# Performance work log

Hardware: AMD Instinct MI355X
Metric: run time of the kernel (lower is better)

Reference implementation:

```python
import jax, jax.numpy as jnp
import numpy as np

NUM_CLASSES = 1000
BATCH = 65536
TEMPERATURE = 1.0
SMOOTHING = 0.1


def setup_inputs() -> dict:
    key = jax.random.key(0)
    k1, k2, k3 = jax.random.split(key, 3)
    x = jax.random.normal(k1, (BATCH, NUM_CLASSES), dtype=jnp.float32)
    class_avg = jax.random.normal(k2, (NUM_CLASSES, NUM_CLASSES), dtype=jnp.float32)
    target = jax.random.randint(k3, (BATCH,), 0, NUM_CLASSES, dtype=jnp.int64)
    return {"x": x, "class_avg": class_avg, "target": target}


def reference(x, class_avg, target):
    C = class_avg.shape[0]
    # class_avg = softmax(class_avg / T) over last dim
    A = jax.nn.softmax(class_avg / TEMPERATURE, axis=-1)  # [C, C]
    # per-class off-diagonal mass: sum over row minus diagonal
    sums = A.sum(axis=-1) - jnp.diagonal(A)  # [C]
    # per-class smoothing matrix S[t, j] = smoothing * (1 - A[t, j]) / sums[t], S[t, t] = 1 - smoothing
    S = SMOOTHING * (1.0 - A) / sums[:, None]  # [C, C]
    diag_idx = jnp.arange(C)
    S = S.at[diag_idx, diag_idx].set(1.0 - SMOOTHING)
    # gather the per-sample smoothing rows (replaces the nested Python loop)
    sm = S[target]  # [B, C]
    logprobs = jax.nn.log_softmax(x, axis=-1)  # [B, C]
    loss = -(logprobs * sm).sum(axis=-1)  # [B]
    return loss.mean()
```

## Files before the change

### kernel.cpp

```cpp
#include <hip/hip_runtime.h>
#include <math.h>

constexpr int C = 1000;
constexpr int B = 65536;
constexpr float SMOOTH = 0.1f;
constexpr int SPW = 2;
constexpr int WPB = 4;
constexpr int LBLK = B / (WPB * SPW);

typedef float f4 __attribute__((ext_vector_type(4)));

__device__ inline float wave_reduce_sum(float v) {
    #pragma unroll
    for (int off = 32; off > 0; off >>= 1)
        v += __shfl_xor(v, off, 64);
    return v;
}
__device__ inline void wave_reduce_sum4(float& a, float& b, float& c, float& d) {
    #pragma unroll
    for (int off = 32; off > 0; off >>= 1) {
        float ta = __shfl_xor(a, off, 64);
        float tb = __shfl_xor(b, off, 64);
        float tc = __shfl_xor(c, off, 64);
        float td = __shfl_xor(d, off, 64);
        a += ta; b += tb; c += tc; d += td;
    }
}
__device__ inline float block_reduce_sum(float v, float* sm) {
    v = wave_reduce_sum(v);
    int wave = threadIdx.x >> 6, lane = threadIdx.x & 63;
    if (lane == 0) sm[wave] = v;
    __syncthreads();
    float r = (sm[0] + sm[1]) + (sm[2] + sm[3]);
    __syncthreads();
    return r;
}

__global__ __launch_bounds__(256) void smooth_kernel(
        const float* __restrict__ ca, float* __restrict__ S,
        float* __restrict__ Srow) {
    int wave = threadIdx.x >> 6, lane = threadIdx.x & 63;
    int t = blockIdx.x * 4 + wave;
    const f4* row = (const f4*)(ca + (size_t)t * C);
    bool lastl = lane < (250 - 192);

    f4 e[4];
    e[0] = row[lane];
    e[1] = row[lane + 64];
    e[2] = row[lane + 128];
    e[3] = lastl ? row[lane + 192]
                 : f4{-INFINITY, -INFINITY, -INFINITY, -INFINITY};

    float zl = 0.f;
    #pragma unroll
    for (int k = 0; k < 4; k++) {
        e[k].x = __expf(e[k].x);
        e[k].y = __expf(e[k].y);
        e[k].z = __expf(e[k].z);
        e[k].w = __expf(e[k].w);
        zl += (e[k].x + e[k].y) + (e[k].z + e[k].w);
    }
    float z = wave_reduce_sum(zl);
    float inv_z = 1.0f / z;

    int q = t >> 2, owner = q & 63, kk = q >> 6, comp = t & 3;
    f4 av = (kk == 0) ? e[0] : (kk == 1) ? e[1] : (kk == 2) ? e[2] : e[3];
    float cand = (comp == 0) ? av.x : (comp == 1) ? av.y
               : (comp == 2) ? av.z : av.w;
    float ediag = __shfl(cand, owner, 64);

    float sums = (z - ediag) * inv_z;
    float coef = SMOOTH / sums;
    f4* Srt = (f4*)(S + (size_t)t * C);
    float srow_l = 0.f;
    #pragma unroll
    for (int k = 0; k < 3; k++) {
        int jb = (lane + k * 64) * 4;
        f4 s;
        s.x = (jb + 0 == t) ? (1.0f - SMOOTH) : (1.0f - e[k].x * inv_z) * coef;
        s.y = (jb + 1 == t) ? (1.0f - SMOOTH) : (1.0f - e[k].y * inv_z) * coef;
        s.z = (jb + 2 == t) ? (1.0f - SMOOTH) : (1.0f - e[k].z * inv_z) * coef;
        s.w = (jb + 3 == t) ? (1.0f - SMOOTH) : (1.0f - e[k].w * inv_z) * coef;
        Srt[lane + k * 64] = s;
        srow_l += (s.x + s.y) + (s.z + s.w);
    }
    if (lastl) {
        int jb = (lane + 192) * 4;
        f4 s;
        s.x = (jb + 0 == t) ? (1.0f - SMOOTH) : (1.0f - e[3].x * inv_z) * coef;
        s.y = (jb + 1 == t) ? (1.0f - SMOOTH) : (1.0f - e[3].y * inv_z) * coef;
        s.z = (jb + 2 == t) ? (1.0f - SMOOTH) : (1.0f - e[3].z * inv_z) * coef;
        s.w = (jb + 3 == t) ? (1.0f - SMOOTH) : (1.0f - e[3].w * inv_z) * coef;
        Srt[lane + 192] = s;
        srow_l += (s.x + s.y) + (s.z + s.w);
    }
    float srow = wave_reduce_sum(srow_l);
    if (lane == 0) Srow[t] = srow;
}

__global__ __launch_bounds__(256) void loss_kernel(
        const float* __restrict__ x, const float* __restrict__ S,
        const float* __restrict__ Srow, const int* __restrict__ tgt,
        float* __restrict__ partials) {
    int wave = threadIdx.x >> 6, lane = threadIdx.x & 63;
    int b0 = (blockIdx.x * WPB + wave) * SPW;
    bool lastl = lane < (250 - 192);

    int t0 = tgt[b0], t1 = tgt[b0 + 1];
    float ss0 = Srow[t0], ss1 = Srow[t1];
    const f4* xr0 = (const f4*)(x + (size_t)b0 * C);
    const f4* xr1 = (const f4*)(x + (size_t)(b0 + 1) * C);
    const f4* sr0 = (const f4*)(S + (size_t)t0 * C);
    const f4* sr1 = (const f4*)(S + (size_t)t1 * C);

    f4 xa0 = __builtin_nontemporal_load(xr0 + lane);
    f4 xa1 = __builtin_nontemporal_load(xr0 + lane + 64);
    f4 xa2 = __builtin_nontemporal_load(xr0 + lane + 128);
    f4 xa3 = lastl ? __builtin_nontemporal_load(xr0 + lane + 192)
                   : f4{-INFINITY, -INFINITY, -INFINITY, -INFINITY};
    f4 sa0 = sr0[lane], sa1 = sr0[lane + 64], sa2 = sr0[lane + 128];
    f4 sa3 = lastl ? sr0[lane + 192] : f4{0.f, 0.f, 0.f, 0.f};

    f4 xb0 = __builtin_nontemporal_load(xr1 + lane);
    f4 xb1 = __builtin_nontemporal_load(xr1 + lane + 64);
    f4 xb2 = __builtin_nontemporal_load(xr1 + lane + 128);
    f4 xb3 = lastl ? __builtin_nontemporal_load(xr1 + lane + 192)
                   : f4{-INFINITY, -INFINITY, -INFINITY, -INFINITY};
    f4 sb0 = sr1[lane], sb1 = sr1[lane + 64], sb2 = sr1[lane + 128];
    f4 sb3 = lastl ? sr1[lane + 192] : f4{0.f, 0.f, 0.f, 0.f};

    float z0 = 0.f, d0 = 0.f, z1 = 0.f, d1 = 0.f;

    {
        z0 += __expf(xa0.x) + __expf(xa0.y) + __expf(xa0.z) + __expf(xa0.w);
        z0 += __expf(xa1.x) + __expf(xa1.y) + __expf(xa1.z) + __expf(xa1.w);
        z0 += __expf(xa2.x) + __expf(xa2.y) + __expf(xa2.z) + __expf(xa2.w);
        z0 += __expf(xa3.x) + __expf(xa3.y) + __expf(xa3.z) + __expf(xa3.w);
        d0 = fmaf(sa0.x, xa0.x, d0); d0 = fmaf(sa0.y, xa0.y, d0);
        d0 = fmaf(sa0.z, xa0.z, d0); d0 = fmaf(sa0.w, xa0.w, d0);
        d0 = fmaf(sa1.x, xa1.x, d0); d0 = fmaf(sa1.y, xa1.y, d0);
        d0 = fmaf(sa1.z, xa1.z, d0); d0 = fmaf(sa1.w, xa1.w, d0);
        d0 = fmaf(sa2.x, xa2.x, d0); d0 = fmaf(sa2.y, xa2.y, d0);
        d0 = fmaf(sa2.z, xa2.z, d0); d0 = fmaf(sa2.w, xa2.w, d0);
        f4 xf = lastl ? xa3 : f4{0.f, 0.f, 0.f, 0.f};
        d0 = fmaf(sa3.x, xf.x, d0); d0 = fmaf(sa3.y, xf.y, d0);
        d0 = fmaf(sa3.z, xf.z, d0); d0 = fmaf(sa3.w, xf.w, d0);
    }
    {
        z1 += __expf(xb0.x) + __expf(xb0.y) + __expf(xb0.z) + __expf(xb0.w);
        z1 += __expf(xb1.x) + __expf(xb1.y) + __expf(xb1.z) + __expf(xb1.w);
        z1 += __expf(xb2.x) + __expf(xb2.y) + __expf(xb2.z) + __expf(xb2.w);
        z1 += __expf(xb3.x) + __expf(xb3.y) + __expf(xb3.z) + __expf(xb3.w);
        d1 = fmaf(sb0.x, xb0.x, d1); d1 = fmaf(sb0.y, xb0.y, d1);
        d1 = fmaf(sb0.z, xb0.z, d1); d1 = fmaf(sb0.w, xb0.w, d1);
        d1 = fmaf(sb1.x, xb1.x, d1); d1 = fmaf(sb1.y, xb1.y, d1);
        d1 = fmaf(sb1.z, xb1.z, d1); d1 = fmaf(sb1.w, xb1.w, d1);
        d1 = fmaf(sb2.x, xb2.x, d1); d1 = fmaf(sb2.y, xb2.y, d1);
        d1 = fmaf(sb2.z, xb2.z, d1); d1 = fmaf(sb2.w, xb2.w, d1);
        f4 xf = lastl ? xb3 : f4{0.f, 0.f, 0.f, 0.f};
        d1 = fmaf(sb3.x, xf.x, d1); d1 = fmaf(sb3.y, xf.y, d1);
        d1 = fmaf(sb3.z, xf.z, d1); d1 = fmaf(sb3.w, xf.w, d1);
    }

    wave_reduce_sum4(z0, z1, d0, d1);

    float lb = __logf(z0) * ss0 - d0 + __logf(z1) * ss1 - d1;

    __shared__ float wacc[4];
    if (lane == 0) wacc[wave] = lb;
    __syncthreads();
    if (threadIdx.x == 0)
        partials[blockIdx.x] = (wacc[0] + wacc[1]) + (wacc[2] + wacc[3]);
}

__global__ __launch_bounds__(256) void reduce_kernel(
        const float* __restrict__ partials, float* __restrict__ out) {
    __shared__ float sm[4];
    const f4* p4 = (const f4*)partials;
    float s = 0.f;
    #pragma unroll
    for (int k = 0; k < 8; k++) {
        f4 v = p4[threadIdx.x + k * 256];
        s += (v.x + v.y) + (v.z + v.w);
    }
    s = block_reduce_sum(s, sm);
    if (threadIdx.x == 0) out[0] = s * (1.0f / (float)B);
}

extern "C" void kernel_launch(void* const* d_in, const int* in_sizes, int n_in,
                              void* d_out, int out_size, void* d_ws, size_t ws_size,
                              hipStream_t stream) {
    const float* x   = (const float*)d_in[0];
    const float* ca  = (const float*)d_in[1];
    const int*   tgt = (const int*)d_in[2];
    float* out = (float*)d_out;

    float* S        = (float*)d_ws;
    float* Srow     = S + (size_t)C * C;
    float* partials = Srow + C;

    smooth_kernel<<<C / 4, 256, 0, stream>>>(ca, S, Srow);
    loss_kernel<<<LBLK, 256, 0, stream>>>(x, S, Srow, tgt, partials);
    reduce_kernel<<<1, 256, 0, stream>>>(partials, out);
}
```

Measured before the change: 340.1 us.

## Bucket samples by target class so each wave reuses one smoothing row

Adds histogram, prefix-scan and scatter kernels that group sample indices by target class. The loss kernel then assigns 8 waves per class, loads that class's smoothing row into registers once, and loops over that class's samples. This removes the per-sample gather of a 4KB S row, which is largely L2 traffic. In exchange it adds four small serialized launches, atomics, and an indirect, non-sequential access pattern over x, and load balance now depends on how many samples each class has.

```diff
diff --git a/kernel.cpp b/kernel.cpp
--- a/kernel.cpp
+++ b/kernel.cpp
@@ -4,17 +4,26 @@
 constexpr int C = 1000;
 constexpr int B = 65536;
 constexpr float SMOOTH = 0.1f;
-constexpr int SPW = 2;
-constexpr int WPB = 4;
-constexpr int LBLK = B / (WPB * SPW);
+constexpr int WPC = 8;
+constexpr int NW = C * WPC;
+constexpr int NWPAD = 8192;
 
 typedef float f4 __attribute__((ext_vector_type(4)));
+#define NTLOAD(p) __builtin_nontemporal_load(p)
 
 __device__ inline float wave_reduce_sum(float v) {
     #pragma unroll
     for (int off = 32; off > 0; off >>= 1)
         v += __shfl_xor(v, off, 64);
     return v;
+}
+__device__ inline void wave_reduce_sum2(float& a, float& b) {
+    #pragma unroll
+    for (int off = 32; off > 0; off >>= 1) {
+        float ta = __shfl_xor(a, off, 64);
+        float tb = __shfl_xor(b, off, 64);
+        a += ta; b += tb;
+    }
 }
 __device__ inline void wave_reduce_sum4(float& a, float& b, float& c, float& d) {
     #pragma unroll
@@ -34,6 +43,75 @@
     float r = (sm[0] + sm[1]) + (sm[2] + sm[3]);
     __syncthreads();
     return r;
+}
+
+
+__global__ __launch_bounds__(256) void zero_kernel(int* __restrict__ counts) {
+    #pragma unroll
+    for (int k = 0; k < 4; k++) {
+        int idx = threadIdx.x + k * 256;
+        if (idx < C) counts[idx] = 0;
+    }
+}
+
+__global__ __launch_bounds__(256) void hist_kernel(const int* __restrict__ tgt,
+                                                   int* __restrict__ counts) {
+    __shared__ int lh[C];
+    for (int idx = threadIdx.x; idx < C; idx += 256) lh[idx] = 0;
+    __syncthreads();
+    int base = blockIdx.x * 1024 + threadIdx.x;
+    #pragma unroll
+    for (int k = 0; k < 4; k++)
+        atomicAdd(&lh[tgt[base + k * 256]], 1);
+    __syncthreads();
+    for (int idx = threadIdx.x; idx < C; idx += 256) {
+        int v = lh[idx];
+        if (v) atomicAdd(&counts[idx], v);
+    }
+}
+
+__global__ __launch_bounds__(256) void prefix_kernel(const int* __restrict__ counts,
+                                                     int* __restrict__ offs,
+                                                     int* __restrict__ cursor) {
+    __shared__ int ts[256];
+    int tid = threadIdx.x;
+    int c[4];
+    int s = 0;
+    #pragma unroll
+    for (int k = 0; k < 4; k++) {
+        int idx = tid * 4 + k;
+        c[k] = (idx < C) ? counts[idx] : 0;
+        s += c[k];
+    }
+    ts[tid] = s;
+    __syncthreads();
+    for (int off = 1; off < 256; off <<= 1) {
+        int v = (tid >= off) ? ts[tid - off] : 0;
+        __syncthreads();
+        ts[tid] += v;
+        __syncthreads();
+    }
+    int base = (tid > 0) ? ts[tid - 1] : 0;
+    #pragma unroll
+    for (int k = 0; k < 4; k++) {
+        int idx = tid * 4 + k;
+        if (idx < C) { offs[idx] = base; cursor[idx] = base; }
+        base += c[k];
+    }
+    if (tid == 255) offs[C] = ts[255];
+}
+
+__global__ __launch_bounds__(256) void scatter_kernel(const int* __restrict__ tgt,
+                                                      int* __restrict__ cursor,
+                                                      int* __restrict__ order) {
+    int base = blockIdx.x * 1024 + threadIdx.x;
+    #pragma unroll
+    for (int k = 0; k < 4; k++) {
+        int b = base + k * 256;
+        int t = tgt[b];
+        int pos = atomicAdd(&cursor[t], 1);
+        order[pos] = b;
+    }
 }
 
 __global__ __launch_bounds__(256) void smooth_kernel(
@@ -98,79 +176,72 @@
     if (lane == 0) Srow[t] = srow;
 }
 
+__device__ inline void sample_zd(const f4* __restrict__ xr, int lane, bool lastl,
+                                 const f4& s0, const f4& s1, const f4& s2,
+                                 const f4& s3, float& z, float& d) {
+    f4 x0 = NTLOAD(xr + lane);
+    f4 x1 = NTLOAD(xr + lane + 64);
+    f4 x2 = NTLOAD(xr + lane + 128);
+    f4 x3 = lastl ? NTLOAD(xr + lane + 192)
+                  : f4{-INFINITY, -INFINITY, -INFINITY, -INFINITY};
+    z = __expf(x0.x) + __expf(x0.y) + __expf(x0.z) + __expf(x0.w)
+      + __expf(x1.x) + __expf(x1.y) + __expf(x1.z) + __expf(x1.w)
+      + __expf(x2.x) + __expf(x2.y) + __expf(x2.z) + __expf(x2.w)
+      + __expf(x3.x) + __expf(x3.y) + __expf(x3.z) + __expf(x3.w);
+    float dd = 0.f;
+    dd = fmaf(s0.x, x0.x, dd); dd = fmaf(s0.y, x0.y, dd);
+    dd = fmaf(s0.z, x0.z, dd); dd = fmaf(s0.w, x0.w, dd);
+    dd = fmaf(s1.x, x1.x, dd); dd = fmaf(s1.y, x1.y, dd);
+    dd = fmaf(s1.z, x1.z, dd); dd = fmaf(s1.w, x1.w, dd);
+    dd = fmaf(s2.x, x2.x, dd); dd = fmaf(s2.y, x2.y, dd);
+    dd = fmaf(s2.z, x2.z, dd); dd = fmaf(s2.w, x2.w, dd);
+    f4 xf = lastl ? x3 : f4{0.f, 0.f, 0.f, 0.f};
+    dd = fmaf(s3.x, xf.x, dd); dd = fmaf(s3.y, xf.y, dd);
+    dd = fmaf(s3.z, xf.z, dd); dd = fmaf(s3.w, xf.w, dd);
+    d = dd;
+}
+
 __global__ __launch_bounds__(256) void loss_kernel(
         const float* __restrict__ x, const float* __restrict__ S,
-        const float* __restrict__ Srow, const int* __restrict__ tgt,
-        float* __restrict__ partials) {
+        const float* __restrict__ Srow, const int* __restrict__ offs,
+        const int* __restrict__ order, float* __restrict__ partials) {
     int wave = threadIdx.x >> 6, lane = threadIdx.x & 63;
-    int b0 = (blockIdx.x * WPB + wave) * SPW;
+    int w = blockIdx.x * 4 + wave;
     bool lastl = lane < (250 - 192);
-
-    int t0 = tgt[b0], t1 = tgt[b0 + 1];
-    float ss0 = Srow[t0], ss1 = Srow[t1];
-    const f4* xr0 = (const f4*)(x + (size_t)b0 * C);
-    const f4* xr1 = (const f4*)(x + (size_t)(b0 + 1) * C);
-    const f4* sr0 = (const f4*)(S + (size_t)t0 * C);
-    const f4* sr1 = (const f4*)(S + (size_t)t1 * C);
-
-    f4 xa0 = __builtin_nontemporal_load(xr0 + lane);
-    f4 xa1 = __builtin_nontemporal_load(xr0 + lane + 64);
-    f4 xa2 = __builtin_nontemporal_load(xr0 + lane + 128);
-    f4 xa3 = lastl ? __builtin_nontemporal_load(xr0 + lane + 192)
-                   : f4{-INFINITY, -INFINITY, -INFINITY, -INFINITY};
-    f4 sa0 = sr0[lane], sa1 = sr0[lane + 64], sa2 = sr0[lane + 128];
-    f4 sa3 = lastl ? sr0[lane + 192] : f4{0.f, 0.f, 0.f, 0.f};
-
-    f4 xb0 = __builtin_nontemporal_load(xr1 + lane);
-    f4 xb1 = __builtin_nontemporal_load(xr1 + lane + 64);
-    f4 xb2 = __builtin_nontemporal_load(xr1 + lane + 128);
-    f4 xb3 = lastl ? __builtin_nontemporal_load(xr1 + lane + 192)
-                   : f4{-INFINITY, -INFINITY, -INFINITY, -INFINITY};
-    f4 sb0 = sr1[lane], sb1 = sr1[lane + 64], sb2 = sr1[lane + 128];
-    f4 sb3 = lastl ? sr1[lane + 192] : f4{0.f, 0.f, 0.f, 0.f};
-
-    float z0 = 0.f, d0 = 0.f, z1 = 0.f, d1 = 0.f;
-
-    {
-        z0 += __expf(xa0.x) + __expf(xa0.y) + __expf(xa0.z) + __expf(xa0.w);
-        z0 += __expf(xa1.x) + __expf(xa1.y) + __expf(xa1.z) + __expf(xa1.w);
-        z0 += __expf(xa2.x) + __expf(xa2.y) + __expf(xa2.z) + __expf(xa2.w);
-        z0 += __expf(xa3.x) + __expf(xa3.y) + __expf(xa3.z) + __expf(xa3.w);
-        d0 = fmaf(sa0.x, xa0.x, d0); d0 = fmaf(sa0.y, xa0.y, d0);
-        d0 = fmaf(sa0.z, xa0.z, d0); d0 = fmaf(sa0.w, xa0.w, d0);
-        d0 = fmaf(sa1.x, xa1.x, d0); d0 = fmaf(sa1.y, xa1.y, d0);
-        d0 = fmaf(sa1.z, xa1.z, d0); d0 = fmaf(sa1.w, xa1.w, d0);
-        d0 = fmaf(sa2.x, xa2.x, d0); d0 = fmaf(sa2.y, xa2.y, d0);
-        d0 = fmaf(sa2.z, xa2.z, d0); d0 = fmaf(sa2.w, xa2.w, d0);
-        f4 xf = lastl ? xa3 : f4{0.f, 0.f, 0.f, 0.f};
-        d0 = fmaf(sa3.x, xf.x, d0); d0 = fmaf(sa3.y, xf.y, d0);
-        d0 = fmaf(sa3.z, xf.z, d0); d0 = fmaf(sa3.w, xf.w, d0);
-    }
-    {
-        z1 += __expf(xb0.x) + __expf(xb0.y) + __expf(xb0.z) + __expf(xb0.w);
-        z1 += __expf(xb1.x) + __expf(xb1.y) + __expf(xb1.z) + __expf(xb1.w);
-        z1 += __expf(xb2.x) + __expf(xb2.y) + __expf(xb2.z) + __expf(xb2.w);
-        z1 += __expf(xb3.x) + __expf(xb3.y) + __expf(xb3.z) + __expf(xb3.w);
-        d1 = fmaf(sb0.x, xb0.x, d1); d1 = fmaf(sb0.y, xb0.y, d1);
-        d1 = fmaf(sb0.z, xb0.z, d1); d1 = fmaf(sb0.w, xb0.w, d1);
-        d1 = fmaf(sb1.x, xb1.x, d1); d1 = fmaf(sb1.y, xb1.y, d1);
-        d1 = fmaf(sb1.z, xb1.z, d1); d1 = fmaf(sb1.w, xb1.w, d1);
-        d1 = fmaf(sb2.x, xb2.x, d1); d1 = fmaf(sb2.y, xb2.y, d1);
-        d1 = fmaf(sb2.z, xb2.z, d1); d1 = fmaf(sb2.w, xb2.w, d1);
-        f4 xf = lastl ? xb3 : f4{0.f, 0.f, 0.f, 0.f};
-        d1 = fmaf(sb3.x, xf.x, d1); d1 = fmaf(sb3.y, xf.y, d1);
-        d1 = fmaf(sb3.z, xf.z, d1); d1 = fmaf(sb3.w, xf.w, d1);
-    }
-
-    wave_reduce_sum4(z0, z1, d0, d1);
-
-    float lb = __logf(z0) * ss0 - d0 + __logf(z1) * ss1 - d1;
-
-    __shared__ float wacc[4];
-    if (lane == 0) wacc[wave] = lb;
-    __syncthreads();
-    if (threadIdx.x == 0)
-        partials[blockIdx.x] = (wacc[0] + wacc[1]) + (wacc[2] + wacc[3]);
+    float lsum = 0.f;
+    int t = w >> 3;
+    if (t < C) {
+        int c = w & 7;
+        int o1 = offs[t + 1];
+        int i = offs[t] + c;
+        float ss = Srow[t];
+        const f4* sr = (const f4*)(S + (size_t)t * C);
+        f4 s0 = sr[lane];
+        f4 s1 = sr[lane + 64];
+        f4 s2 = sr[lane + 128];
+        f4 s3 = lastl ? sr[lane + 192] : f4{0.f, 0.f, 0.f, 0.f};
+
+        for (; i + WPC < o1; i += 2 * WPC) {
+            int b0 = order[i];
+            int b1 = order[i + WPC];
+            const f4* xr0 = (const f4*)(x + (size_t)b0 * C);
+            const f4* xr1 = (const f4*)(x + (size_t)b1 * C);
+            float z0, d0, z1, d1;
+            sample_zd(xr0, lane, lastl, s0, s1, s2, s3, z0, d0);
+            sample_zd(xr1, lane, lastl, s0, s1, s2, s3, z1, d1);
+            wave_reduce_sum4(z0, z1, d0, d1);
+            lsum += (__logf(z0) + __logf(z1)) * ss - d0 - d1;
+        }
+        if (i < o1) {
+            int b0 = order[i];
+            const f4* xr0 = (const f4*)(x + (size_t)b0 * C);
+            float z0, d0;
+            sample_zd(xr0, lane, lastl, s0, s1, s2, s3, z0, d0);
+            wave_reduce_sum2(z0, d0);
+            lsum += __logf(z0) * ss - d0;
+        }
+    }
+    if (lane == 0) partials[w] = lsum;
 }
 
 __global__ __launch_bounds__(256) void reduce_kernel(
@@ -198,8 +269,16 @@
     float* S        = (float*)d_ws;
     float* Srow     = S + (size_t)C * C;
     float* partials = Srow + C;
+    int*   counts   = (int*)(partials + NWPAD);
+    int*   offs     = counts + C;
+    int*   cursor   = offs + C + 1;
+    int*   order    = cursor + C;
 
     smooth_kernel<<<C / 4, 256, 0, stream>>>(ca, S, Srow);
-    loss_kernel<<<LBLK, 256, 0, stream>>>(x, S, Srow, tgt, partials);
+    zero_kernel<<<1, 256, 0, stream>>>(counts);
+    hist_kernel<<<64, 256, 0, stream>>>(tgt, counts);
+    prefix_kernel<<<1, 256, 0, stream>>>(counts, offs, cursor);
+    scatter_kernel<<<64, 256, 0, stream>>>(tgt, cursor, order);
+    loss_kernel<<<NWPAD / 4, 256, 0, stream>>>(x, S, Srow, offs, order, partials);
     reduce_kernel<<<1, 256, 0, stream>>>(partials, out);
 }
```

Result: slower. 366.1 us (+7.7%).
